# Kernel optimization log

Hardware: AMD Instinct MI355X
Metric: run time of the kernel (lower is better)

## Reference

```python
import jax, jax.numpy as jnp
import numpy as np

B, D_IN, D_FEAT = 256, 512, 512   # batch, encoder in-dim, encoder out-dim (= Sender input_dim)
H, V, E, L = 512, 32000, 64, 16   # hidden_size, vocab_size, embedding_dim, length


def setup_inputs() -> dict:
    key = jax.random.key(0)
    ks = jax.random.split(key, 12)
    s = lambda *d: 1.0 / np.sqrt(d[-1])
    return {
        "x": jax.random.normal(ks[0], (B, D_IN), jnp.float32),
        # encoder: Linear(D_IN, D_FEAT)
        "enc_W": jax.random.normal(ks[1], (D_FEAT, D_IN), jnp.float32) * s(D_IN),
        "enc_b": jnp.zeros((D_FEAT,), jnp.float32),
        # input_layer: Linear(D_FEAT, H)
        "in_W": jax.random.normal(ks[2], (H, D_FEAT), jnp.float32) * s(D_FEAT),
        "in_b": jnp.zeros((H,), jnp.float32),
        # GRU cell (torch layout: gates ordered r, z, n)
        "W_ih": jax.random.normal(ks[3], (3 * H, E), jnp.float32) * s(H),
        "W_hh": jax.random.normal(ks[4], (3 * H, H), jnp.float32) * s(H),
        "b_ih": jnp.zeros((3 * H,), jnp.float32),
        "b_hh": jnp.zeros((3 * H,), jnp.float32),
        # output_layer: Linear(H, V)
        "out_W": jax.random.normal(ks[5], (V, H), jnp.float32) * s(H),
        "out_b": jnp.zeros((V,), jnp.float32),
        # msg_embedding table and sos embedding parameter
        "emb_table": jax.random.normal(ks[6], (V, E), jnp.float32),
        "sos_emb": jax.random.normal(ks[7], (E,), jnp.float32),
    }


def _gru_cell(e, h, W_ih, W_hh, b_ih, b_hh):
    gi = e @ W_ih.T + b_ih            # [B, 3H]
    gh = h @ W_hh.T + b_hh            # [B, 3H]
    gi_r, gi_z, gi_n = jnp.split(gi, 3, axis=-1)
    gh_r, gh_z, gh_n = jnp.split(gh, 3, axis=-1)
    r = jax.nn.sigmoid(gi_r + gh_r)
    z = jax.nn.sigmoid(gi_z + gh_z)
    n = jnp.tanh(gi_n + r * gh_n)
    return (1.0 - z) * n + z * h


def reference(x, enc_W, enc_b, in_W, in_b, W_ih, W_hh, b_ih, b_hh,
              out_W, out_b, emb_table, sos_emb):
    # encoder -> input_layer -> initial hidden state (num_layers = 1)
    feat = x @ enc_W.T + enc_b                  # [B, D_FEAT]
    h0 = feat @ in_W.T + in_b                   # [B, H]
    e0 = jnp.broadcast_to(sos_emb, (x.shape[0], E))  # sos embedding repeated over batch

    def step(carry, _):
        h, e = carry
        h = _gru_cell(e, h, W_ih, W_hh, b_ih, b_hh)      # [B, H]
        logits_t = h @ out_W.T + out_b                    # [B, V]
        sym = jnp.argmax(logits_t, axis=-1)               # eval-mode greedy symbol [B]
        e_next = emb_table[sym]                           # [B, E]
        return (h, e_next), (sym, logits_t)

    (_, _), (syms, logits) = jax.lax.scan(step, (h0, e0), None, length=L)
    sequence = syms.T                                     # [B, L] int
    logits = jnp.transpose(logits, (1, 0, 2))             # [B, L, V]
    return sequence, logits
```

## Files before the change

### kernel.cpp

```cpp
#include <hip/hip_runtime.h>
#include <math.h>

#define BATCH 256
#define DIN 512
#define DFEAT 512
#define HSZ 512
#define VOCAB 32000
#define EMB 64
#define SLEN 16
#define NTILE 500
#define MARGIN 0.0625f

typedef __attribute__((ext_vector_type(8))) short bf16x8;
typedef __attribute__((ext_vector_type(4))) float f32x4;

__device__ inline unsigned bf16_rne(float x) {
    union { float f; unsigned u; } u; u.f = x;
    unsigned r = u.u + 0x7fff + ((u.u >> 16) & 1);
    return r >> 16;
}

template<int BM, int BN, int BK, int TM, int TN>
__global__ __launch_bounds__(256) void gemm_atb(
    const float* __restrict__ A,
    const float* __restrict__ W,
    const float* __restrict__ bias,
    float* __restrict__ C, long long ldc,
    int M, int N, int K)
{
    __shared__ float As[BK][BM + 4];
    __shared__ float Bs[BK][BN + 4];
    constexpr int THREADS = (BM / TM) * (BN / TN);
    const int tid = threadIdx.x;
    const int tx = tid % (BN / TN);
    const int ty = tid / (BN / TN);
    const int row0 = blockIdx.y * BM;
    const int col0 = blockIdx.x * BN;
    float acc[TM][TN] = {};
    for (int k0 = 0; k0 < K; k0 += BK) {
        for (int i = tid; i < BM * BK; i += THREADS) {
            int m = i / BK, k = i % BK;
            As[k][m] = A[(long long)(row0 + m) * K + k0 + k];
        }
        for (int i = tid; i < BN * BK; i += THREADS) {
            int n = i / BK, k = i % BK;
            Bs[k][n] = W[(long long)(col0 + n) * K + k0 + k];
        }
        __syncthreads();
        #pragma unroll
        for (int kk = 0; kk < BK; ++kk) {
            float a[TM], b[TN];
            #pragma unroll
            for (int i = 0; i < TM; ++i) a[i] = As[kk][ty * TM + i];
            #pragma unroll
            for (int j = 0; j < TN; ++j) b[j] = Bs[kk][tx * TN + j];
            #pragma unroll
            for (int i = 0; i < TM; ++i)
                #pragma unroll
                for (int j = 0; j < TN; ++j)
                    acc[i][j] = fmaf(a[i], b[j], acc[i][j]);
        }
        __syncthreads();
    }
    #pragma unroll
    for (int i = 0; i < TM; ++i) {
        long long m = row0 + ty * TM + i;
        float* crow = C + m * ldc;
        #pragma unroll
        for (int j = 0; j < TN; ++j) {
            int n = col0 + tx * TN + j;
            float v = acc[i][j];
            if (bias) v += bias[n];
            crow[n] = v;
        }
    }
}

__global__ void prep_kernel(const float* __restrict__ out_W, ushort* __restrict__ Wb,
                            const float* __restrict__ W_ih, const float* __restrict__ W_hh,
                            const float* __restrict__ b_ih, const float* __restrict__ b_hh,
                            float* __restrict__ Wcat2, float* __restrict__ bcat2,
                            int* __restrict__ done)
{
    const int stride = gridDim.x * 256;
    const int t0 = blockIdx.x * 256 + threadIdx.x;
    for (int i = t0; i < VOCAB * HSZ / 4; i += stride) {
        const float4 v = ((const float4*)out_W)[i];
        ushort4 o;
        o.x = (ushort)bf16_rne(v.x); o.y = (ushort)bf16_rne(v.y);
        o.z = (ushort)bf16_rne(v.z); o.w = (ushort)bf16_rne(v.w);
        ((ushort4*)Wb)[i] = o;
    }
    for (long long i = t0; i < 2048LL * 576; i += stride) {
        int g = (int)(i / 576), k = (int)(i % 576);
        int j = g >> 2, comp = g & 3;
        float v;
        if (comp == 0)      v = (k < 64) ? W_ih[j * 64 + k]          : W_hh[(long long)j * 512 + k - 64];
        else if (comp == 1) v = (k < 64) ? W_ih[(512 + j) * 64 + k]  : W_hh[(long long)(512 + j) * 512 + k - 64];
        else if (comp == 2) v = (k < 64) ? W_ih[(1024 + j) * 64 + k] : 0.f;
        else                v = (k < 64) ? 0.f                        : W_hh[(long long)(1024 + j) * 512 + k - 64];
        Wcat2[i] = v;
    }
    for (int i = t0; i < 2048; i += stride) {
        int j = i >> 2, comp = i & 3;
        float bv = (comp == 0) ? b_ih[j] + b_hh[j]
                 : (comp == 1) ? b_ih[512 + j] + b_hh[512 + j]
                 : (comp == 2) ? b_ih[1024 + j] : b_hh[1024 + j];
        bcat2[i] = bv;
    }
    if (t0 == 0) *done = 0;
}

template<bool FIRST>
__global__ __launch_bounds__(256) void ag2_kernel(
    const float* __restrict__ hprev, float* __restrict__ hnew,
    const float* __restrict__ Wcat2, const float* __restrict__ bcat2,
    float* __restrict__ ebuf, const float* __restrict__ sos,
    ushort* __restrict__ hbf,
    const float* __restrict__ tmaxv, const float* __restrict__ lprev,
    const float* __restrict__ out_W, const float* __restrict__ out_b,
    const float* __restrict__ emb, float* __restrict__ seq,
    int* __restrict__ done, int wait_target, int tprev)
{
    __shared__ __align__(16) char smem[22528];
    __shared__ float s_red[256];
    __shared__ int s_qt[64];
    __shared__ int s_cand[64];
    __shared__ float s_rv[64];
    __shared__ int s_cnt2[2];
    __shared__ int s_sym;
    const int tid = threadIdx.x;
    const int lane = tid & 63, wave = tid >> 6;
    const int blk = blockIdx.x;

    if (!FIRST && blk < BATCH) {
        const int b = blk;
        const float* row = lprev + (long long)b * (SLEN * (long long)VOCAB);
        float v0 = tmaxv[(long long)b * 512 + tid];
        float v1 = (tid + 256 < NTILE) ? tmaxv[(long long)b * 512 + 256 + tid] : -INFINITY;
        s_red[tid] = fmaxf(v0, v1); __syncthreads();
        for (int s = 128; s > 0; s >>= 1) {
            if (tid < s) s_red[tid] = fmaxf(s_red[tid], s_red[tid + s]);
            __syncthreads();
        }
        float M = s_red[0];
        if (tid == 0) { s_cnt2[0] = 0; s_cnt2[1] = 0; }
        __syncthreads();
        if (v0 >= M - MARGIN) {
            int s = atomicAdd(&s_cnt2[0], 1);
            if (s < 64) s_qt[s] = tid;
        }
        if (v1 >= M - MARGIN) {
            int s = atomicAdd(&s_cnt2[0], 1);
            if (s < 64) s_qt[s] = tid + 256;
        }
        __syncthreads();
        int nq = min(s_cnt2[0], 64);
        for (int idx = tid; idx < nq * 64; idx += 256) {
            int c = s_qt[idx >> 6] * 64 + (idx & 63);
            if (row[c] >= M - MARGIN) {
                int s = atomicAdd(&s_cnt2[1], 1);
                if (s < 64) s_cand[s] = c;
            }
        }
        __syncthreads();
        int nc = min(s_cnt2[1], 64);
        const float* hrow = hprev + (long long)b * 512;
        for (int ci = wave; ci < nc; ci += 4) {
            int vv = s_cand[ci];
            const float* wrow = out_W + (long long)vv * 512;
            float s = 0.f;
            for (int k = lane; k < 512; k += 64) s = fmaf(hrow[k], wrow[k], s);
            for (int off = 32; off > 0; off >>= 1) s += __shfl_down(s, off, 64);
            if (lane == 0) s_rv[ci] = s + out_b[vv];
        }
        __syncthreads();
        if (tid == 0) {
            float bv = -INFINITY; int sym = 0x7fffffff;
            for (int ci = 0; ci < nc; ++ci) {
                float xx = s_rv[ci]; int c = s_cand[ci];
                if (xx > bv || (xx == bv && c < sym)) { bv = xx; sym = c; }
            }
            if (sym < 0 || sym >= VOCAB) sym = 0;
            seq[b * SLEN + tprev] = (float)sym;
            s_sym = sym;
        }
        __syncthreads();
        if (tid < EMB)
            __hip_atomic_store(&ebuf[(long long)b * EMB + tid],
                               emb[(long long)s_sym * EMB + tid],
                               __ATOMIC_RELAXED, __HIP_MEMORY_SCOPE_AGENT);
        __syncthreads();
        if (tid == 0)
            __hip_atomic_fetch_add(done, 1, __ATOMIC_RELEASE, __HIP_MEMORY_SCOPE_AGENT);
        __syncthreads();
    }

    const int ty = blk >> 5;
    const int tx = blk & 31;
    float* As = (float*)smem;
    float* Bs = (float*)(smem + 4608);
    const int tyt = tid >> 4;
    const int txt = tid & 15;
    float acc[4] = {};

    for (int k0 = 64; k0 < 576; k0 += 64) {
        for (int i = tid; i < 16 * 64; i += 256) {
            int m = i >> 6, k = i & 63;
            As[k * 18 + m] = hprev[(long long)(ty * 16 + m) * 512 + (k0 - 64) + k];
        }
        for (int i = tid; i < 64 * 64; i += 256) {
            int n = i >> 6, k = i & 63;
            Bs[k * 68 + n] = Wcat2[(long long)(tx * 64 + n) * 576 + k0 + k];
        }
        __syncthreads();
        #pragma unroll 8
        for (int kk = 0; kk < 64; ++kk) {
            const float a = As[kk * 18 + tyt];
            const float4 b = *(const float4*)&Bs[kk * 68 + txt * 4];
            acc[0] = fmaf(a, b.x, acc[0]);
            acc[1] = fmaf(a, b.y, acc[1]);
            acc[2] = fmaf(a, b.z, acc[2]);
            acc[3] = fmaf(a, b.w, acc[3]);
        }
        __syncthreads();
    }

    if (!FIRST) {
        if (tid == 0) {
            while (__hip_atomic_load(done, __ATOMIC_RELAXED, __HIP_MEMORY_SCOPE_AGENT) < wait_target)
                __builtin_amdgcn_s_sleep(8);
            __hip_atomic_load(done, __ATOMIC_ACQUIRE, __HIP_MEMORY_SCOPE_AGENT);
        }
        __syncthreads();
    }
    {
        for (int i = tid; i < 16 * 64; i += 256) {
            int m = i >> 6, k = i & 63;
            float v;
            if (FIRST) v = sos[k];
            else v = __hip_atomic_load(&ebuf[(long long)(ty * 16 + m) * EMB + k],
                                       __ATOMIC_RELAXED, __HIP_MEMORY_SCOPE_AGENT);
            As[k * 18 + m] = v;
        }
        for (int i = tid; i < 64 * 64; i += 256) {
            int n = i >> 6, k = i & 63;
            Bs[k * 68 + n] = Wcat2[(long long)(tx * 64 + n) * 576 + k];
        }
        __syncthreads();
        #pragma unroll 8
        for (int kk = 0; kk < 64; ++kk) {
            const float a = As[kk * 18 + tyt];
            const float4 b = *(const float4*)&Bs[kk * 68 + txt * 4];
            acc[0] = fmaf(a, b.x, acc[0]);
            acc[1] = fmaf(a, b.y, acc[1]);
            acc[2] = fmaf(a, b.z, acc[2]);
            acc[3] = fmaf(a, b.w, acc[3]);
        }
        __syncthreads();
    }

    float* gt = (float*)smem;
    #pragma unroll
    for (int j = 0; j < 4; ++j)
        gt[tyt * 64 + txt * 4 + j] = acc[j];
    __syncthreads();
    {
        int row = tid >> 4, jl = tid & 15;
        int jg = tx * 16 + jl;
        float gr  = gt[row * 64 + jl * 4 + 0] + bcat2[jg * 4 + 0];
        float gz  = gt[row * 64 + jl * 4 + 1] + bcat2[jg * 4 + 1];
        float gni = gt[row * 64 + jl * 4 + 2] + bcat2[jg * 4 + 2];
        float gnh = gt[row * 64 + jl * 4 + 3] + bcat2[jg * 4 + 3];
        float r = 1.0f / (1.0f + expf(-gr));
        float z = 1.0f / (1.0f + expf(-gz));
        float n = tanhf(gni + r * gnh);
        long long bglob = ty * 16 + row;
        float hold = hprev[bglob * 512 + jg];
        float h = (1.0f - z) * n + z * hold;
        hnew[bglob * 512 + jg] = h;
        hbf[bglob * 512 + jg] = (ushort)bf16_rne(h);
    }
}

__global__ __launch_bounds__(256) void logits_bm128_kernel(
    const ushort* __restrict__ hbf,
    const ushort* __restrict__ Wb,
    const float* __restrict__ out_b,
    float* __restrict__ lbase, float* __restrict__ tmaxv)
{
    __shared__ __align__(16) char As[16384];
    __shared__ __align__(16) char Bs[8192];
    __shared__ float s_mv[128];
    const int tid = threadIdx.x;
    const int lane = tid & 63;
    const int wave = tid >> 6;
    const int bid = blockIdx.x;
    const int job = (bid & 7) * 125 + (bid >> 3);
    const int jx = job >> 1;
    const int jy = job & 1;
    const int row0 = jy * 128;
    const int col0 = jx * 64;

    f32x4 acc[2][4] = {};
    const int srow = tid >> 3;
    const int sch = tid & 7;

    for (int k0 = 0; k0 < 512; k0 += 64) {
        #pragma unroll
        for (int ra = 0; ra < 4; ++ra) {
            int row = ra * 32 + srow;
            const char* g = (const char*)(hbf + (long long)(row0 + row) * 512 + k0) + ((sch ^ (row & 7)) * 16);
            __builtin_amdgcn_global_load_lds(
                (const __attribute__((address_space(1))) void*)g,
                (__attribute__((address_space(3))) void*)(As + row * 128 + sch * 16), 16, 0, 0);
        }
        #pragma unroll
        for (int rb = 0; rb < 2; ++rb) {
            int row = rb * 32 + srow;
            const char* g = (const char*)(Wb + (long long)(col0 + row) * 512 + k0) + ((sch ^ (row & 7)) * 16);
            __builtin_amdgcn_global_load_lds(
                (const __attribute__((address_space(1))) void*)g,
                (__attribute__((address_space(3))) void*)(Bs + row * 128 + sch * 16), 16, 0, 0);
        }
        __syncthreads();
        #pragma unroll
        for (int k32 = 0; k32 < 64; k32 += 32) {
            bf16x8 af[2], bfr[4];
            #pragma unroll
            for (int f = 0; f < 2; ++f) {
                int rA = wave * 32 + f * 16 + (lane & 15);
                int byteA = (rA * 128 + (k32 + ((lane >> 4) << 3)) * 2) ^ ((rA & 7) << 4);
                af[f] = *(const bf16x8*)&As[byteA];
            }
            #pragma unroll
            for (int j = 0; j < 4; ++j) {
                int rB = j * 16 + (lane & 15);
                int byteB = (rB * 128 + (k32 + ((lane >> 4) << 3)) * 2) ^ ((rB & 7) << 4);
                bfr[j] = *(const bf16x8*)&Bs[byteB];
            }
            #pragma unroll
            for (int f = 0; f < 2; ++f)
                #pragma unroll
                for (int j = 0; j < 4; ++j)
                    acc[f][j] = __builtin_amdgcn_mfma_f32_16x16x32_bf16(af[f], bfr[j], acc[f][j], 0, 0, 0);
        }
        __syncthreads();
    }

    #pragma unroll
    for (int f = 0; f < 2; ++f) {
        #pragma unroll
        for (int q = 0; q < 4; ++q) {
            int r_local = wave * 32 + f * 16 + ((lane >> 4) << 2) + q;
            float* crow = lbase + (long long)(row0 + r_local) * (SLEN * (long long)VOCAB);
            float mv = -INFINITY;
            #pragma unroll
            for (int j = 0; j < 4; ++j) {
                int c = col0 + j * 16 + (lane & 15);
                float v = acc[f][j][q] + out_b[c];
                __builtin_nontemporal_store(v, &crow[c]);
                mv = fmaxf(mv, v);
            }
            #pragma unroll
            for (int m = 1; m < 16; m <<= 1) mv = fmaxf(mv, __shfl_xor(mv, m, 64));
            if ((lane & 15) == 0) s_mv[r_local] = mv;
        }
    }
    __syncthreads();
    if (tid < 128)
        tmaxv[(long long)(row0 + tid) * 512 + jx] = s_mv[tid];
}

__global__ __launch_bounds__(256) void argmax_kernel(
    const float* __restrict__ tmaxv, const float* __restrict__ lbase,
    const float* __restrict__ h, const float* __restrict__ out_W,
    const float* __restrict__ out_b, const float* __restrict__ emb,
    float* __restrict__ seq, float* __restrict__ ebuf, int t)
{
    __shared__ float s_red[256];
    __shared__ int s_qt[64];
    __shared__ int s_cand[64];
    __shared__ float s_rv[64];
    __shared__ int s_cnt2[2];
    __shared__ int s_sym;
    const int b = blockIdx.x;
    const int tid = threadIdx.x;
    const int lane = tid & 63, wave = tid >> 6;
    const float* row = lbase + (long long)b * (SLEN * (long long)VOCAB);

    float v0 = tmaxv[(long long)b * 512 + tid];
    float v1 = (tid + 256 < NTILE) ? tmaxv[(long long)b * 512 + 256 + tid] : -INFINITY;
    s_red[tid] = fmaxf(v0, v1); __syncthreads();
    for (int s = 128; s > 0; s >>= 1) {
        if (tid < s) s_red[tid] = fmaxf(s_red[tid], s_red[tid + s]);
        __syncthreads();
    }
    float M = s_red[0];
    if (tid == 0) { s_cnt2[0] = 0; s_cnt2[1] = 0; }
    __syncthreads();
    if (v0 >= M - MARGIN) {
        int s = atomicAdd(&s_cnt2[0], 1);
        if (s < 64) s_qt[s] = tid;
    }
    if (v1 >= M - MARGIN) {
        int s = atomicAdd(&s_cnt2[0], 1);
        if (s < 64) s_qt[s] = tid + 256;
    }
    __syncthreads();
    int nq = min(s_cnt2[0], 64);
    for (int idx = tid; idx < nq * 64; idx += 256) {
        int c = s_qt[idx >> 6] * 64 + (idx & 63);
        if (row[c] >= M - MARGIN) {
            int s = atomicAdd(&s_cnt2[1], 1);
            if (s < 64) s_cand[s] = c;
        }
    }
    __syncthreads();
    int nc = min(s_cnt2[1], 64);
    const float* hrow = h + (long long)b * 512;
    for (int ci = wave; ci < nc; ci += 4) {
        int vv = s_cand[ci];
        const float* wrow = out_W + (long long)vv * 512;
        float s = 0.f;
        for (int k = lane; k < 512; k += 64) s = fmaf(hrow[k], wrow[k], s);
        for (int off = 32; off > 0; off >>= 1) s += __shfl_down(s, off, 64);
        if (lane == 0) s_rv[ci] = s + out_b[vv];
    }
    __syncthreads();
    if (tid == 0) {
        float bv = -INFINITY; int sym = 0x7fffffff;
        for (int ci = 0; ci < nc; ++ci) {
            float xx = s_rv[ci]; int c = s_cand[ci];
            if (xx > bv || (xx == bv && c < sym)) { bv = xx; sym = c; }
        }
        if (sym < 0 || sym >= VOCAB) sym = 0;
        seq[b * SLEN + t] = (float)sym;
        s_sym = sym;
    }
    __syncthreads();
    if (tid < EMB) ebuf[(long long)b * EMB + tid] = emb[(long long)s_sym * EMB + tid];
}

extern "C" void kernel_launch(void* const* d_in, const int* in_sizes, int n_in,
                              void* d_out, int out_size, void* d_ws, size_t ws_size,
                              hipStream_t stream) {
    const float* x     = (const float*)d_in[0];
    const float* enc_W = (const float*)d_in[1];
    const float* enc_b = (const float*)d_in[2];
    const float* in_W  = (const float*)d_in[3];
    const float* in_b  = (const float*)d_in[4];
    const float* W_ih  = (const float*)d_in[5];
    const float* W_hh  = (const float*)d_in[6];
    const float* b_ih  = (const float*)d_in[7];
    const float* b_hh  = (const float*)d_in[8];
    const float* out_W = (const float*)d_in[9];
    const float* out_b = (const float*)d_in[10];
    const float* emb   = (const float*)d_in[11];
    const float* sos   = (const float*)d_in[12];

    float* seq    = (float*)d_out;
    float* logits = (float*)d_out + BATCH * SLEN;

    char* p = (char*)d_ws;
    ushort* Wb    = (ushort*)p;  p += (size_t)VOCAB * HSZ * 2;
    float* Wcat2  = (float*)p;   p += (size_t)2048 * 576 * 4;
    float* bcat2  = (float*)p;   p += 2048 * 4;
    float* hA     = (float*)p;   p += (size_t)BATCH * HSZ * 4;
    float* hB     = (float*)p;   p += (size_t)BATCH * HSZ * 4;
    ushort* hbf   = (ushort*)p;  p += (size_t)BATCH * HSZ * 2;
    float* ebuf   = (float*)p;   p += (size_t)BATCH * EMB * 4;
    float* feat   = (float*)p;   p += (size_t)BATCH * DFEAT * 4;
    float* tmaxv  = (float*)p;   p += (size_t)BATCH * 512 * 4;
    int*   done   = (int*)p;     p += 64;

    prep_kernel<<<1024, 256, 0, stream>>>(out_W, Wb, W_ih, W_hh, b_ih, b_hh,
                                          Wcat2, bcat2, done);
    gemm_atb<64, 64, 32, 4, 4><<<dim3(DFEAT / 64, BATCH / 64), 256, 0, stream>>>(
        x, enc_W, enc_b, feat, DFEAT, BATCH, DFEAT, DIN);
    gemm_atb<64, 64, 32, 4, 4><<<dim3(HSZ / 64, BATCH / 64), 256, 0, stream>>>(
        feat, in_W, in_b, hA, HSZ, BATCH, HSZ, DFEAT);

    float* hc = hA;
    float* hn = hB;
    for (int t = 0; t < SLEN; ++t) {
        float* lbase = logits + (long long)t * VOCAB;
        if (t == 0) {
            ag2_kernel<true><<<512, 256, 0, stream>>>(
                hc, hn, Wcat2, bcat2, ebuf, sos, hbf,
                tmaxv, logits, out_W, out_b, emb, seq, done, 0, 0);
        } else {
            ag2_kernel<false><<<512, 256, 0, stream>>>(
                hc, hn, Wcat2, bcat2, ebuf, sos, hbf,
                tmaxv, logits + (long long)(t - 1) * VOCAB,
                out_W, out_b, emb, seq, done, 256 * t, t - 1);
        }
        logits_bm128_kernel<<<1000, 256, 0, stream>>>(hbf, Wb, out_b, lbase, tmaxv);
        float* tmp = hc; hc = hn; hn = tmp;
    }
    argmax_kernel<<<BATCH, 256, 0, stream>>>(
        tmaxv, logits + (long long)(SLEN - 1) * VOCAB, hc, out_W, out_b, emb,
        seq, ebuf, SLEN - 1);
}
```

Before: 1.150 ms.

## Merge GRU step and logits GEMM into one persistent-style kernel with device flags

Fuses the per-step GRU/argmax kernel and the logits MFMA GEMM into a single 1000-block launch. The first 512 blocks compute the GRU and publish bf16 hidden state via atomic stores plus a release counter, and all blocks spin on that counter before running the logits tile. This removes one kernel launch and its boundary per step and lets logits blocks start as soon as the hidden state is ready. It depends on all blocks being co-resident, which is checked with an occupancy query and falls back to the two-kernel path otherwise. Spin-waiting can deadlock or waste CU time if residency assumptions fail.

```diff
diff --git a/kernel.cpp b/kernel.cpp
--- a/kernel.cpp
+++ b/kernel.cpp
@@ -108,98 +108,177 @@
                  : (comp == 2) ? b_ih[1024 + j] : b_hh[1024 + j];
         bcat2[i] = bv;
     }
-    if (t0 == 0) *done = 0;
-}
-
-template<bool FIRST>
-__global__ __launch_bounds__(256) void ag2_kernel(
+    if (t0 == 0) { done[0] = 0; done[8] = 0; }
+}
+
+
+__device__ __forceinline__ int argmax_body(int b, int tprev,
+    const float* __restrict__ tmaxv, const float* __restrict__ lprev,
+    const float* __restrict__ hprev, const float* __restrict__ out_W,
+    const float* __restrict__ out_b, float* __restrict__ seq, char* sm)
+{
+    float* s_red = (float*)sm;
+    int*   s_qt  = (int*)(sm + 1024);
+    int*   s_cand= (int*)(sm + 1280);
+    float* s_rv  = (float*)(sm + 1536);
+    int*   s_cnt = (int*)(sm + 1792);
+    int*   s_sym = (int*)(sm + 1800);
+    const int tid = threadIdx.x;
+    const int lane = tid & 63, wave = tid >> 6;
+    const float* row = lprev + (long long)b * (SLEN * (long long)VOCAB);
+
+    float v0 = tmaxv[(long long)b * 512 + tid];
+    float v1 = (tid + 256 < NTILE) ? tmaxv[(long long)b * 512 + 256 + tid] : -INFINITY;
+    s_red[tid] = fmaxf(v0, v1); __syncthreads();
+    for (int s = 128; s > 0; s >>= 1) {
+        if (tid < s) s_red[tid] = fmaxf(s_red[tid], s_red[tid + s]);
+        __syncthreads();
+    }
+    float M = s_red[0];
+    if (tid == 0) { s_cnt[0] = 0; s_cnt[1] = 0; }
+    __syncthreads();
+    if (v0 >= M - MARGIN) {
+        int s = atomicAdd(&s_cnt[0], 1);
+        if (s < 64) s_qt[s] = tid;
+    }
+    if (v1 >= M - MARGIN) {
+        int s = atomicAdd(&s_cnt[0], 1);
+        if (s < 64) s_qt[s] = tid + 256;
+    }
+    __syncthreads();
+    int nq = min(s_cnt[0], 64);
+    for (int idx = tid; idx < nq * 64; idx += 256) {
+        int c = s_qt[idx >> 6] * 64 + (idx & 63);
+        if (row[c] >= M - MARGIN) {
+            int s = atomicAdd(&s_cnt[1], 1);
+            if (s < 64) s_cand[s] = c;
+        }
+    }
+    __syncthreads();
+    int nc = min(s_cnt[1], 64);
+    const float* hrow = hprev + (long long)b * 512;
+    for (int ci = wave; ci < nc; ci += 4) {
+        int vv = s_cand[ci];
+        const float* wrow = out_W + (long long)vv * 512;
+        float s = 0.f;
+        for (int k = lane; k < 512; k += 64) s = fmaf(hrow[k], wrow[k], s);
+        for (int off = 32; off > 0; off >>= 1) s += __shfl_down(s, off, 64);
+        if (lane == 0) s_rv[ci] = s + out_b[vv];
+    }
+    __syncthreads();
+    if (tid == 0) {
+        float bv = -INFINITY; int sym = 0x7fffffff;
+        for (int ci = 0; ci < nc; ++ci) {
+            float xx = s_rv[ci]; int c = s_cand[ci];
+            if (xx > bv || (xx == bv && c < sym)) { bv = xx; sym = c; }
+        }
+        if (sym < 0 || sym >= VOCAB) sym = 0;
+        seq[b * SLEN + tprev] = (float)sym;
+        *s_sym = sym;
+    }
+    __syncthreads();
+    return *s_sym;
+}
+
+__device__ __forceinline__ void logits_body(int bid,
+    const ushort* __restrict__ hbf, const ushort* __restrict__ Wb,
+    const float* __restrict__ out_b, float* __restrict__ lbase,
+    float* __restrict__ tmaxv, char* sm)
+{
+    char* As = sm;
+    char* Bs = sm + 16384;
+    float* s_mv = (float*)(sm + 24576);
+    const int tid = threadIdx.x;
+    const int lane = tid & 63;
+    const int wave = tid >> 6;
+    const int job = (bid & 7) * 125 + (bid >> 3);
+    const int jx = job >> 1;
+    const int jy = job & 1;
+    const int row0 = jy * 128;
+    const int col0 = jx * 64;
+
+    f32x4 acc[2][4] = {};
+    const int srow = tid >> 3;
+    const int sch = tid & 7;
+
+    for (int k0 = 0; k0 < 512; k0 += 64) {
+        #pragma unroll
+        for (int ra = 0; ra < 4; ++ra) {
+            int row = ra * 32 + srow;
+            const char* g = (const char*)(hbf + (long long)(row0 + row) * 512 + k0) + ((sch ^ (row & 7)) * 16);
+            __builtin_amdgcn_global_load_lds(
+                (const __attribute__((address_space(1))) void*)g,
+                (__attribute__((address_space(3))) void*)(As + row * 128 + sch * 16), 16, 0, 0);
+        }
+        #pragma unroll
+        for (int rb = 0; rb < 2; ++rb) {
+            int row = rb * 32 + srow;
+            const char* g = (const char*)(Wb + (long long)(col0 + row) * 512 + k0) + ((sch ^ (row & 7)) * 16);
+            __builtin_amdgcn_global_load_lds(
+                (const __attribute__((address_space(1))) void*)g,
+                (__attribute__((address_space(3))) void*)(Bs + row * 128 + sch * 16), 16, 0, 0);
+        }
+        __syncthreads();
+        #pragma unroll
+        for (int k32 = 0; k32 < 64; k32 += 32) {
+            bf16x8 af[2], bfr[4];
+            #pragma unroll
+            for (int f = 0; f < 2; ++f) {
+                int rA = wave * 32 + f * 16 + (lane & 15);
+                int byteA = (rA * 128 + (k32 + ((lane >> 4) << 3)) * 2) ^ ((rA & 7) << 4);
+                af[f] = *(const bf16x8*)&As[byteA];
+            }
+            #pragma unroll
+            for (int j = 0; j < 4; ++j) {
+                int rB = j * 16 + (lane & 15);
+                int byteB = (rB * 128 + (k32 + ((lane >> 4) << 3)) * 2) ^ ((rB & 7) << 4);
+                bfr[j] = *(const bf16x8*)&Bs[byteB];
+            }
+            #pragma unroll
+            for (int f = 0; f < 2; ++f)
+                #pragma unroll
+                for (int j = 0; j < 4; ++j)
+                    acc[f][j] = __builtin_amdgcn_mfma_f32_16x16x32_bf16(af[f], bfr[j], acc[f][j], 0, 0, 0);
+        }
+        __syncthreads();
+    }
+
+    #pragma unroll
+    for (int f = 0; f < 2; ++f) {
+        #pragma unroll
+        for (int q = 0; q < 4; ++q) {
+            int r_local = wave * 32 + f * 16 + ((lane >> 4) << 2) + q;
+            float* crow = lbase + (long long)(row0 + r_local) * (SLEN * (long long)VOCAB);
+            float mv = -INFINITY;
+            #pragma unroll
+            for (int j = 0; j < 4; ++j) {
+                int c = col0 + j * 16 + (lane & 15);
+                float v = acc[f][j][q] + out_b[c];
+                __builtin_nontemporal_store(v, &crow[c]);
+                mv = fmaxf(mv, v);
+            }
+            #pragma unroll
+            for (int m = 1; m < 16; m <<= 1) mv = fmaxf(mv, __shfl_xor(mv, m, 64));
+            if ((lane & 15) == 0) s_mv[r_local] = mv;
+        }
+    }
+    __syncthreads();
+    if (tid < 128)
+        tmaxv[(long long)(row0 + tid) * 512 + jx] = s_mv[tid];
+}
+
+template<bool FIRST, bool MERGED>
+__device__ __forceinline__ void gru_body(int blk,
     const float* __restrict__ hprev, float* __restrict__ hnew,
     const float* __restrict__ Wcat2, const float* __restrict__ bcat2,
     float* __restrict__ ebuf, const float* __restrict__ sos,
-    ushort* __restrict__ hbf,
-    const float* __restrict__ tmaxv, const float* __restrict__ lprev,
-    const float* __restrict__ out_W, const float* __restrict__ out_b,
-    const float* __restrict__ emb, float* __restrict__ seq,
-    int* __restrict__ done, int wait_target, int tprev)
-{
-    __shared__ __align__(16) char smem[22528];
-    __shared__ float s_red[256];
-    __shared__ int s_qt[64];
-    __shared__ int s_cand[64];
-    __shared__ float s_rv[64];
-    __shared__ int s_cnt2[2];
-    __shared__ int s_sym;
+    unsigned* __restrict__ hbfu, int* __restrict__ done, int wt_e, char* sm)
+{
     const int tid = threadIdx.x;
-    const int lane = tid & 63, wave = tid >> 6;
-    const int blk = blockIdx.x;
-
-    if (!FIRST && blk < BATCH) {
-        const int b = blk;
-        const float* row = lprev + (long long)b * (SLEN * (long long)VOCAB);
-        float v0 = tmaxv[(long long)b * 512 + tid];
-        float v1 = (tid + 256 < NTILE) ? tmaxv[(long long)b * 512 + 256 + tid] : -INFINITY;
-        s_red[tid] = fmaxf(v0, v1); __syncthreads();
-        for (int s = 128; s > 0; s >>= 1) {
-            if (tid < s) s_red[tid] = fmaxf(s_red[tid], s_red[tid + s]);
-            __syncthreads();
-        }
-        float M = s_red[0];
-        if (tid == 0) { s_cnt2[0] = 0; s_cnt2[1] = 0; }
-        __syncthreads();
-        if (v0 >= M - MARGIN) {
-            int s = atomicAdd(&s_cnt2[0], 1);
-            if (s < 64) s_qt[s] = tid;
-        }
-        if (v1 >= M - MARGIN) {
-            int s = atomicAdd(&s_cnt2[0], 1);
-            if (s < 64) s_qt[s] = tid + 256;
-        }
-        __syncthreads();
-        int nq = min(s_cnt2[0], 64);
-        for (int idx = tid; idx < nq * 64; idx += 256) {
-            int c = s_qt[idx >> 6] * 64 + (idx & 63);
-            if (row[c] >= M - MARGIN) {
-                int s = atomicAdd(&s_cnt2[1], 1);
-                if (s < 64) s_cand[s] = c;
-            }
-        }
-        __syncthreads();
-        int nc = min(s_cnt2[1], 64);
-        const float* hrow = hprev + (long long)b * 512;
-        for (int ci = wave; ci < nc; ci += 4) {
-            int vv = s_cand[ci];
-            const float* wrow = out_W + (long long)vv * 512;
-            float s = 0.f;
-            for (int k = lane; k < 512; k += 64) s = fmaf(hrow[k], wrow[k], s);
-            for (int off = 32; off > 0; off >>= 1) s += __shfl_down(s, off, 64);
-            if (lane == 0) s_rv[ci] = s + out_b[vv];
-        }
-        __syncthreads();
-        if (tid == 0) {
-            float bv = -INFINITY; int sym = 0x7fffffff;
-            for (int ci = 0; ci < nc; ++ci) {
-                float xx = s_rv[ci]; int c = s_cand[ci];
-                if (xx > bv || (xx == bv && c < sym)) { bv = xx; sym = c; }
-            }
-            if (sym < 0 || sym >= VOCAB) sym = 0;
-            seq[b * SLEN + tprev] = (float)sym;
-            s_sym = sym;
-        }
-        __syncthreads();
-        if (tid < EMB)
-            __hip_atomic_store(&ebuf[(long long)b * EMB + tid],
-                               emb[(long long)s_sym * EMB + tid],
-                               __ATOMIC_RELAXED, __HIP_MEMORY_SCOPE_AGENT);
-        __syncthreads();
-        if (tid == 0)
-            __hip_atomic_fetch_add(done, 1, __ATOMIC_RELEASE, __HIP_MEMORY_SCOPE_AGENT);
-        __syncthreads();
-    }
-
     const int ty = blk >> 5;
     const int tx = blk & 31;
-    float* As = (float*)smem;
-    float* Bs = (float*)(smem + 4608);
+    float* As = (float*)sm;
+    float* Bs = (float*)(sm + 4608);
     const int tyt = tid >> 4;
     const int txt = tid & 15;
     float acc[4] = {};
@@ -228,9 +307,9 @@
 
     if (!FIRST) {
         if (tid == 0) {
-            while (__hip_atomic_load(done, __ATOMIC_RELAXED, __HIP_MEMORY_SCOPE_AGENT) < wait_target)
+            while (__hip_atomic_load(&done[0], __ATOMIC_RELAXED, __HIP_MEMORY_SCOPE_AGENT) < wt_e)
                 __builtin_amdgcn_s_sleep(8);
-            __hip_atomic_load(done, __ATOMIC_ACQUIRE, __HIP_MEMORY_SCOPE_AGENT);
+            __hip_atomic_load(&done[0], __ATOMIC_ACQUIRE, __HIP_MEMORY_SCOPE_AGENT);
         }
         __syncthreads();
     }
@@ -260,7 +339,8 @@
         __syncthreads();
     }
 
-    float* gt = (float*)smem;
+    float* gt = (float*)sm;
+    ushort* sh_hb = (ushort*)(sm + 8192);
     #pragma unroll
     for (int j = 0; j < 4; ++j)
         gt[tyt * 64 + txt * 4 + j] = acc[j];
@@ -279,167 +359,111 @@
         float hold = hprev[bglob * 512 + jg];
         float h = (1.0f - z) * n + z * hold;
         hnew[bglob * 512 + jg] = h;
-        hbf[bglob * 512 + jg] = (ushort)bf16_rne(h);
-    }
+        sh_hb[row * 16 + jl] = (ushort)bf16_rne(h);
+    }
+    __syncthreads();
+    if (tid < 128) {
+        int row = tid >> 3, jp = tid & 7;
+        unsigned lo = sh_hb[row * 16 + jp * 2];
+        unsigned hi = sh_hb[row * 16 + jp * 2 + 1];
+        unsigned v = (hi << 16) | lo;
+        long long idx = (long long)(ty * 16 + row) * 256 + tx * 8 + jp;
+        if (MERGED)
+            __hip_atomic_store(&hbfu[idx], v, __ATOMIC_RELAXED, __HIP_MEMORY_SCOPE_AGENT);
+        else
+            hbfu[idx] = v;
+    }
+    if (MERGED) {
+        __syncthreads();
+        if (tid == 0)
+            __hip_atomic_fetch_add(&done[8], 1, __ATOMIC_RELEASE, __HIP_MEMORY_SCOPE_AGENT);
+    }
+}
+
+template<bool FIRST>
+__global__ __launch_bounds__(256) void gl_kernel(
+    const float* __restrict__ hprev, float* __restrict__ hnew,
+    const float* __restrict__ Wcat2, const float* __restrict__ bcat2,
+    float* __restrict__ ebuf, const float* __restrict__ sos,
+    unsigned* __restrict__ hbfu, const ushort* __restrict__ Wb,
+    const float* __restrict__ out_W, const float* __restrict__ out_b,
+    const float* __restrict__ emb, float* __restrict__ seq,
+    float* __restrict__ tmaxv, const float* __restrict__ lprev,
+    float* __restrict__ lbase, int* __restrict__ done,
+    int wt_e, int wt_l, int tprev)
+{
+    __shared__ __align__(16) char smem[25600];
+    const int tid = threadIdx.x;
+    const int bid = blockIdx.x;
+
+    if (!FIRST && bid < BATCH) {
+        int sym = argmax_body(bid, tprev, tmaxv, lprev, hprev, out_W, out_b, seq, smem);
+        if (tid < EMB)
+            __hip_atomic_store(&ebuf[(long long)bid * EMB + tid],
+                               emb[(long long)sym * EMB + tid],
+                               __ATOMIC_RELAXED, __HIP_MEMORY_SCOPE_AGENT);
+        __syncthreads();
+        if (tid == 0)
+            __hip_atomic_fetch_add(&done[0], 1, __ATOMIC_RELEASE, __HIP_MEMORY_SCOPE_AGENT);
+        __syncthreads();
+    }
+
+    if (bid < 512)
+        gru_body<FIRST, true>(bid, hprev, hnew, Wcat2, bcat2, ebuf, sos, hbfu, done, wt_e, smem);
+
+    if (tid == 0) {
+        while (__hip_atomic_load(&done[8], __ATOMIC_RELAXED, __HIP_MEMORY_SCOPE_AGENT) < wt_l)
+            __builtin_amdgcn_s_sleep(8);
+        __hip_atomic_load(&done[8], __ATOMIC_ACQUIRE, __HIP_MEMORY_SCOPE_AGENT);
+    }
+    __syncthreads();
+    logits_body(bid, (const ushort*)hbfu, Wb, out_b, lbase, tmaxv, smem);
+}
+
+template<bool FIRST>
+__global__ __launch_bounds__(256) void ag2_kernel(
+    const float* __restrict__ hprev, float* __restrict__ hnew,
+    const float* __restrict__ Wcat2, const float* __restrict__ bcat2,
+    float* __restrict__ ebuf, const float* __restrict__ sos,
+    unsigned* __restrict__ hbfu,
+    const float* __restrict__ tmaxv, const float* __restrict__ lprev,
+    const float* __restrict__ out_W, const float* __restrict__ out_b,
+    const float* __restrict__ emb, float* __restrict__ seq,
+    int* __restrict__ done, int wt_e, int tprev)
+{
+    __shared__ __align__(16) char smem[25600];
+    const int tid = threadIdx.x;
+    const int bid = blockIdx.x;
+    if (!FIRST && bid < BATCH) {
+        int sym = argmax_body(bid, tprev, tmaxv, lprev, hprev, out_W, out_b, seq, smem);
+        if (tid < EMB)
+            __hip_atomic_store(&ebuf[(long long)bid * EMB + tid],
+                               emb[(long long)sym * EMB + tid],
+                               __ATOMIC_RELAXED, __HIP_MEMORY_SCOPE_AGENT);
+        __syncthreads();
+        if (tid == 0)
+            __hip_atomic_fetch_add(&done[0], 1, __ATOMIC_RELEASE, __HIP_MEMORY_SCOPE_AGENT);
+        __syncthreads();
+    }
+    gru_body<FIRST, false>(bid, hprev, hnew, Wcat2, bcat2, ebuf, sos, hbfu, done, wt_e, smem);
 }
 
 __global__ __launch_bounds__(256) void logits_bm128_kernel(
-    const ushort* __restrict__ hbf,
-    const ushort* __restrict__ Wb,
+    const ushort* __restrict__ hbf, const ushort* __restrict__ Wb,
     const float* __restrict__ out_b,
     float* __restrict__ lbase, float* __restrict__ tmaxv)
 {
-    __shared__ __align__(16) char As[16384];
-    __shared__ __align__(16) char Bs[8192];
-    __shared__ float s_mv[128];
-    const int tid = threadIdx.x;
-    const int lane = tid & 63;
-    const int wave = tid >> 6;
-    const int bid = blockIdx.x;
-    const int job = (bid & 7) * 125 + (bid >> 3);
-    const int jx = job >> 1;
-    const int jy = job & 1;
-    const int row0 = jy * 128;
-    const int col0 = jx * 64;
-
-    f32x4 acc[2][4] = {};
-    const int srow = tid >> 3;
-    const int sch = tid & 7;
-
-    for (int k0 = 0; k0 < 512; k0 += 64) {
-        #pragma unroll
-        for (int ra = 0; ra < 4; ++ra) {
-            int row = ra * 32 + srow;
-            const char* g = (const char*)(hbf + (long long)(row0 + row) * 512 + k0) + ((sch ^ (row & 7)) * 16);
-            __builtin_amdgcn_global_load_lds(
-                (const __attribute__((address_space(1))) void*)g,
-                (__attribute__((address_space(3))) void*)(As + row * 128 + sch * 16), 16, 0, 0);
-        }
-        #pragma unroll
-        for (int rb = 0; rb < 2; ++rb) {
-            int row = rb * 32 + srow;
-            const char* g = (const char*)(Wb + (long long)(col0 + row) * 512 + k0) + ((sch ^ (row & 7)) * 16);
-            __builtin_amdgcn_global_load_lds(
-                (const __attribute__((address_space(1))) void*)g,
-                (__attribute__((address_space(3))) void*)(Bs + row * 128 + sch * 16), 16, 0, 0);
-        }
-        __syncthreads();
-        #pragma unroll
-        for (int k32 = 0; k32 < 64; k32 += 32) {
-            bf16x8 af[2], bfr[4];
-            #pragma unroll
-            for (int f = 0; f < 2; ++f) {
-                int rA = wave * 32 + f * 16 + (lane & 15);
-                int byteA = (rA * 128 + (k32 + ((lane >> 4) << 3)) * 2) ^ ((rA & 7) << 4);
-                af[f] = *(const bf16x8*)&As[byteA];
-            }
-            #pragma unroll
-            for (int j = 0; j < 4; ++j) {
-                int rB = j * 16 + (lane & 15);
-                int byteB = (rB * 128 + (k32 + ((lane >> 4) << 3)) * 2) ^ ((rB & 7) << 4);
-                bfr[j] = *(const bf16x8*)&Bs[byteB];
-            }
-            #pragma unroll
-            for (int f = 0; f < 2; ++f)
-                #pragma unroll
-                for (int j = 0; j < 4; ++j)
-                    acc[f][j] = __builtin_amdgcn_mfma_f32_16x16x32_bf16(af[f], bfr[j], acc[f][j], 0, 0, 0);
-        }
-        __syncthreads();
-    }
-
-    #pragma unroll
-    for (int f = 0; f < 2; ++f) {
-        #pragma unroll
-        for (int q = 0; q < 4; ++q) {
-            int r_local = wave * 32 + f * 16 + ((lane >> 4) << 2) + q;
-            float* crow = lbase + (long long)(row0 + r_local) * (SLEN * (long long)VOCAB);
-            float mv = -INFINITY;
-            #pragma unroll
-            for (int j = 0; j < 4; ++j) {
-                int c = col0 + j * 16 + (lane & 15);
-                float v = acc[f][j][q] + out_b[c];
-                __builtin_nontemporal_store(v, &crow[c]);
-                mv = fmaxf(mv, v);
-            }
-            #pragma unroll
-            for (int m = 1; m < 16; m <<= 1) mv = fmaxf(mv, __shfl_xor(mv, m, 64));
-            if ((lane & 15) == 0) s_mv[r_local] = mv;
-        }
-    }
-    __syncthreads();
-    if (tid < 128)
-        tmaxv[(long long)(row0 + tid) * 512 + jx] = s_mv[tid];
-}
-
-__global__ __launch_bounds__(256) void argmax_kernel(
+    __shared__ __align__(16) char smem[25600];
+    logits_body(blockIdx.x, hbf, Wb, out_b, lbase, tmaxv, smem);
+}
+
+__global__ __launch_bounds__(256) void argmax_final(
     const float* __restrict__ tmaxv, const float* __restrict__ lbase,
     const float* __restrict__ h, const float* __restrict__ out_W,
-    const float* __restrict__ out_b, const float* __restrict__ emb,
-    float* __restrict__ seq, float* __restrict__ ebuf, int t)
-{
-    __shared__ float s_red[256];
-    __shared__ int s_qt[64];
-    __shared__ int s_cand[64];
-    __shared__ float s_rv[64];
-    __shared__ int s_cnt2[2];
-    __shared__ int s_sym;
-    const int b = blockIdx.x;
-    const int tid = threadIdx.x;
-    const int lane = tid & 63, wave = tid >> 6;
-    const float* row = lbase + (long long)b * (SLEN * (long long)VOCAB);
-
-    float v0 = tmaxv[(long long)b * 512 + tid];
-    float v1 = (tid + 256 < NTILE) ? tmaxv[(long long)b * 512 + 256 + tid] : -INFINITY;
-    s_red[tid] = fmaxf(v0, v1); __syncthreads();
-    for (int s = 128; s > 0; s >>= 1) {
-        if (tid < s) s_red[tid] = fmaxf(s_red[tid], s_red[tid + s]);
-        __syncthreads();
-    }
-    float M = s_red[0];
-    if (tid == 0) { s_cnt2[0] = 0; s_cnt2[1] = 0; }
-    __syncthreads();
-    if (v0 >= M - MARGIN) {
-        int s = atomicAdd(&s_cnt2[0], 1);
-        if (s < 64) s_qt[s] = tid;
-    }
-    if (v1 >= M - MARGIN) {
-        int s = atomicAdd(&s_cnt2[0], 1);
-        if (s < 64) s_qt[s] = tid + 256;
-    }
-    __syncthreads();
-    int nq = min(s_cnt2[0], 64);
-    for (int idx = tid; idx < nq * 64; idx += 256) {
-        int c = s_qt[idx >> 6] * 64 + (idx & 63);
-        if (row[c] >= M - MARGIN) {
-            int s = atomicAdd(&s_cnt2[1], 1);
-            if (s < 64) s_cand[s] = c;
-        }
-    }
-    __syncthreads();
-    int nc = min(s_cnt2[1], 64);
-    const float* hrow = h + (long long)b * 512;
-    for (int ci = wave; ci < nc; ci += 4) {
-        int vv = s_cand[ci];
-        const float* wrow = out_W + (long long)vv * 512;
-        float s = 0.f;
-        for (int k = lane; k < 512; k += 64) s = fmaf(hrow[k], wrow[k], s);
-        for (int off = 32; off > 0; off >>= 1) s += __shfl_down(s, off, 64);
-        if (lane == 0) s_rv[ci] = s + out_b[vv];
-    }
-    __syncthreads();
-    if (tid == 0) {
-        float bv = -INFINITY; int sym = 0x7fffffff;
-        for (int ci = 0; ci < nc; ++ci) {
-            float xx = s_rv[ci]; int c = s_cand[ci];
-            if (xx > bv || (xx == bv && c < sym)) { bv = xx; sym = c; }
-        }
-        if (sym < 0 || sym >= VOCAB) sym = 0;
-        seq[b * SLEN + t] = (float)sym;
-        s_sym = sym;
-    }
-    __syncthreads();
-    if (tid < EMB) ebuf[(long long)b * EMB + tid] = emb[(long long)s_sym * EMB + tid];
+    const float* __restrict__ out_b, float* __restrict__ seq, int t)
+{
+    __shared__ __align__(16) char smem[2048];
+    argmax_body(blockIdx.x, t, tmaxv, lbase, h, out_W, out_b, seq, smem);
 }
 
 extern "C" void kernel_launch(void* const* d_in, const int* in_sizes, int n_in,
@@ -468,7 +492,7 @@
     float* bcat2  = (float*)p;   p += 2048 * 4;
     float* hA     = (float*)p;   p += (size_t)BATCH * HSZ * 4;
     float* hB     = (float*)p;   p += (size_t)BATCH * HSZ * 4;
-    ushort* hbf   = (ushort*)p;  p += (size_t)BATCH * HSZ * 2;
+    unsigned* hbfu= (unsigned*)p; p += (size_t)BATCH * HSZ * 2;
     float* ebuf   = (float*)p;   p += (size_t)BATCH * EMB * 4;
     float* feat   = (float*)p;   p += (size_t)BATCH * DFEAT * 4;
     float* tmaxv  = (float*)p;   p += (size_t)BATCH * 512 * 4;
@@ -481,24 +505,41 @@
     gemm_atb<64, 64, 32, 4, 4><<<dim3(HSZ / 64, BATCH / 64), 256, 0, stream>>>(
         feat, in_W, in_b, hA, HSZ, BATCH, HSZ, DFEAT);
 
+    int nb = 0;
+    hipError_t qerr = hipOccupancyMaxActiveBlocksPerMultiprocessor(
+        &nb, reinterpret_cast<const void*>(gl_kernel<false>), 256, 0);
+    bool merged = (qerr == hipSuccess && nb >= 4);
+
     float* hc = hA;
     float* hn = hB;
     for (int t = 0; t < SLEN; ++t) {
         float* lbase = logits + (long long)t * VOCAB;
-        if (t == 0) {
-            ag2_kernel<true><<<512, 256, 0, stream>>>(
-                hc, hn, Wcat2, bcat2, ebuf, sos, hbf,
-                tmaxv, logits, out_W, out_b, emb, seq, done, 0, 0);
+        const float* lprev = logits + (long long)(t > 0 ? t - 1 : 0) * VOCAB;
+        if (merged) {
+            if (t == 0) {
+                gl_kernel<true><<<1000, 256, 0, stream>>>(
+                    hc, hn, Wcat2, bcat2, ebuf, sos, hbfu, Wb, out_W, out_b, emb, seq,
+                    tmaxv, lprev, lbase, done, 0, 512, 0);
+            } else {
+                gl_kernel<false><<<1000, 256, 0, stream>>>(
+                    hc, hn, Wcat2, bcat2, ebuf, sos, hbfu, Wb, out_W, out_b, emb, seq,
+                    tmaxv, lprev, lbase, done, 256 * t, 512 * (t + 1), t - 1);
+            }
         } else {
-            ag2_kernel<false><<<512, 256, 0, stream>>>(
-                hc, hn, Wcat2, bcat2, ebuf, sos, hbf,
-                tmaxv, logits + (long long)(t - 1) * VOCAB,
-                out_W, out_b, emb, seq, done, 256 * t, t - 1);
-        }
-        logits_bm128_kernel<<<1000, 256, 0, stream>>>(hbf, Wb, out_b, lbase, tmaxv);
+            if (t == 0) {
+                ag2_kernel<true><<<512, 256, 0, stream>>>(
+                    hc, hn, Wcat2, bcat2, ebuf, sos, hbfu,
+                    tmaxv, lprev, out_W, out_b, emb, seq, done, 0, 0);
+            } else {
+                ag2_kernel<false><<<512, 256, 0, stream>>>(
+                    hc, hn, Wcat2, bcat2, ebuf, sos, hbfu,
+                    tmaxv, lprev, out_W, out_b, emb, seq, done, 256 * t, t - 1);
+            }
+            logits_bm128_kernel<<<1000, 256, 0, stream>>>(
+                (const ushort*)hbfu, Wb, out_b, lbase, tmaxv);
+        }
         float* tmp = hc; hc = hn; hn = tmp;
     }
-    argmax_kernel<<<BATCH, 256, 0, stream>>>(
-        tmaxv, logits + (long long)(SLEN - 1) * VOCAB, hc, out_W, out_b, emb,
-        seq, ebuf, SLEN - 1);
-}
+    argmax_final<<<BATCH, 256, 0, stream>>>(
+        tmaxv, logits + (long long)(SLEN - 1) * VOCAB, hc, out_W, out_b, seq, SLEN - 1);
+}
```

Result: no change. 1.155 ms (+0.4%).
